# Performance work log

Measured on AMD Instinct MI355X. Metric: run time of the kernel, lower is better.

Reference implementation:

```python
import jax, jax.numpy as jnp
import numpy as np

N_NODES = 50000
HIDDEN = 256
DEPTH = 6
NUM_GRAPHS = 500


def _build_graph(n):
    # 4-regular directed graph: node i -> (i+1, i-1, i+5, i-5) mod n.
    offs = np.array([1, -1, 5, -5], dtype=np.int64)
    src = np.repeat(np.arange(n, dtype=np.int64), 4)
    dst = (src + np.tile(offs, n)) % n
    # incoming edge ids of node u (edge id = 4*src + offset_index)
    u = np.arange(n, dtype=np.int64)
    incoming = np.stack([4 * ((u - 1) % n) + 0,
                         4 * ((u + 1) % n) + 1,
                         4 * ((u - 5) % n) + 2,
                         4 * ((u + 5) % n) + 3], axis=1)  # [n,4]
    E = 4 * n
    pred = incoming[src]           # [E,4] candidate line-graph predecessors of edge e
    pred_src = pred // 4           # source node of each predecessor edge
    keep = pred_src != dst[:, None]  # drop backtracking edge (exactly 1 per row)
    lg_src = pred[keep]                                   # [3E]
    lg_dst = np.repeat(np.arange(E, dtype=np.int64), 4)[keep.ravel()]  # [3E]
    return src, dst, lg_src, lg_dst


def setup_inputs() -> dict:
    key = jax.random.key(0)
    ks = jax.random.split(key, 8)
    n, H = N_NODES, HIDDEN
    E = 4 * n
    _, dst, lg_src, lg_dst = _build_graph(n)
    graph_ids = np.arange(n, dtype=np.int64) // (n // NUM_GRAPHS)
    s = 0.02  # small weight scale keeps relu message passing stable over DEPTH iters
    return {
        "x_nodes": jax.random.normal(ks[0], (n, 35), jnp.float32),
        "x_edges": jax.random.normal(ks[1], (E, 40), jnp.float32),
        "t_m": jax.random.normal(ks[2], (E, H), jnp.float32) * 0.1,
        "W_i": jax.random.normal(ks[3], (40, H), jnp.float32) * s,
        "W_h": jax.random.normal(ks[4], (H, H), jnp.float32) * s,
        "W_o": jax.random.normal(ks[5], (35 + H, H), jnp.float32) * s,
        "b_o": jax.random.normal(ks[6], (H,), jnp.float32) * s,
        "edge_dst": jnp.asarray(dst, jnp.int32),
        "lg_src": jnp.asarray(lg_src, jnp.int32),
        "lg_dst": jnp.asarray(lg_dst, jnp.int32),
        "graph_ids": jnp.asarray(graph_ids, jnp.int32),
        "num_graphs": NUM_GRAPHS,
    }


def reference(x_nodes, x_edges, t_m, W_i, W_h, W_o, b_o,
              edge_dst, lg_src, lg_dst, graph_ids, num_graphs):
    E = x_edges.shape[0]
    n = x_nodes.shape[0]
    binput = x_edges @ W_i                       # W_i has no bias
    g_m = jax.nn.relu(binput)                    # [E,H] per-edge message
    # tree-message aggregation over line graph is constant across depth iters
    t_agg = jax.ops.segment_sum(t_m[lg_src], lg_dst, num_segments=E)
    for _ in range(DEPTH - 1):
        g_agg = jax.ops.segment_sum(g_m[lg_src], lg_dst, num_segments=E)
        g_m = jax.nn.relu(binput + (g_agg + t_agg) @ W_h)
    # edge -> dst-node aggregation (copy_e + sum)
    nei1 = jax.ops.segment_sum(g_m, edge_dst, num_segments=n)
    nei2 = jax.ops.segment_sum(t_m, edge_dst, num_segments=n)
    ainput = jnp.concatenate([x_nodes, nei1 + nei2], axis=1)  # [n, 35+H]
    atom_hiddens = jax.nn.relu(ainput @ W_o + b_o)
    # dgl.mean_nodes: per-graph mean of node features
    sums = jax.ops.segment_sum(atom_hiddens, graph_ids, num_segments=num_graphs)
    counts = jax.ops.segment_sum(jnp.ones((n, 1), atom_hiddens.dtype), graph_ids,
                                 num_segments=num_graphs)
    return sums / counts
```

## Files before the change

kernel.cpp:

```cpp
#include <hip/hip_runtime.h>


#define H 256

typedef __attribute__((ext_vector_type(4))) float f32x4;
typedef __attribute__((ext_vector_type(8))) short bf16x8;

#define MFMA(a, b, c) __builtin_amdgcn_mfma_f32_16x16x32_bf16((a), (b), (c), 0, 0, 0)

__device__ __forceinline__ float bf2f(ushort u) {
  union { unsigned int i; float f; } v; v.i = ((unsigned int)u) << 16; return v.f;
}
__device__ __forceinline__ ushort f2bf(float f) {
  union { float f; unsigned int i; } v; v.f = f;
  unsigned int i = v.i;
  i += 0x7fffu + ((i >> 16) & 1u);
  return (ushort)(i >> 16);
}

union AFrag { bf16x8 v; ushort u[8]; };

__device__ __forceinline__ int edge_delta(int o) {
  return ((o & 2) ? 5 : 1) * ((o & 1) ? -1 : 1);
}

__device__ __forceinline__ int phi(int L) {
  return (L & ~31) | (((L >> 2) & 1) << 4) | (((L >> 3) & 3) << 2) | (L & 3);
}

__global__ __launch_bounds__(256) void prep_weights_kernel(
    const float* __restrict__ Wh, const float* __restrict__ Wi, const float* __restrict__ Wo,
    ushort* __restrict__ WhF, ushort* __restrict__ WiTF,
    ushort* __restrict__ WoT1, ushort* __restrict__ WoT2) {
  const int nn = blockIdx.x;
  const int t = threadIdx.x;
  const int w = phi(nn);
  const int nfg = w >> 4, l15w = w & 15;
  const int ks = t >> 5, kg = (t >> 3) & 3, i = t & 7;
  WhF[((nfg * 8 + ks) << 9) + ((kg << 4) + l15w) * 8 + i] = f2bf(Wh[t * H + nn]);
  WoT2[nn * H + t] = f2bf(Wo[(35 + t) * H + nn]);
  if (t < 64) {
    WiTF[((nfg * 2 + ks) << 9) + ((kg << 4) + l15w) * 8 + i] =
        (t < 40) ? f2bf(Wi[t * H + nn]) : (ushort)0;
    WoT1[nn * 64 + t] = (t < 35) ? f2bf(Wo[t * H + nn]) : (ushort)0;
  }
}

__global__ __launch_bounds__(256) void sum_tm_kernel(
    const float* __restrict__ t_m, ushort* __restrict__ t3, ushort* __restrict__ t4,
    int n, int useT4) {
  const int idx = blockIdx.x * 256 + threadIdx.x;
  const int s = idx >> 5;
  if (s >= n) return;
  const int cg = (idx & 31) * 8;
  int im1 = s - 1; if (im1 < 0) im1 += n;
  int ip1 = s + 1; if (ip1 >= n) ip1 -= n;
  int im5 = s - 5; if (im5 < 0) im5 += n;
  int ip5 = s + 5; if (ip5 >= n) ip5 -= n;
  const size_t e0 = (size_t)(4 * im1 + 0) * H + cg;
  const size_t e1 = (size_t)(4 * ip1 + 1) * H + cg;
  const size_t e2 = (size_t)(4 * im5 + 2) * H + cg;
  const size_t e3 = (size_t)(4 * ip5 + 3) * H + cg;
  f32x4 v0a = *(const f32x4*)(t_m + e0), v0b = *(const f32x4*)(t_m + e0 + 4);
  f32x4 v1a = *(const f32x4*)(t_m + e1), v1b = *(const f32x4*)(t_m + e1 + 4);
  f32x4 v2a = *(const f32x4*)(t_m + e2), v2b = *(const f32x4*)(t_m + e2 + 4);
  f32x4 v3a = *(const f32x4*)(t_m + e3), v3b = *(const f32x4*)(t_m + e3 + 4);
  f32x4 Sa = v0a + v1a + v2a + v3a;
  f32x4 Sb = v0b + v1b + v2b + v3b;
  f32x4 ra[4] = {Sa - v1a, Sa - v0a, Sa - v3a, Sa - v2a};
  f32x4 rb[4] = {Sb - v1b, Sb - v0b, Sb - v3b, Sb - v2b};
  const int cgs = cg >> 5;
  const int cgk = (cg >> 3) & 3;
#pragma unroll
  for (int o = 0; o < 4; ++o) {
    AFrag a;
#pragma unroll
    for (int i = 0; i < 4; ++i) { a.u[i] = f2bf(ra[o][i]); a.u[4 + i] = f2bf(rb[o][i]); }
    const int e = 4 * s + o;
    *(bf16x8*)(t3 + (((size_t)(e >> 4)) << 12) + (cgs << 9) + (((cgk << 4) + (e & 15)) << 3)) = a.v;
  }
  if (useT4) {
    AFrag a;
#pragma unroll
    for (int i = 0; i < 4; ++i) { a.u[i] = f2bf(Sa[i]); a.u[4 + i] = f2bf(Sb[i]); }
    *(bf16x8*)(t4 + (((size_t)(s >> 4)) << 12) + (cgs << 9) + (((cgk << 4) + (s & 15)) << 3)) = a.v;
  }
}

__global__ __launch_bounds__(1024, 8) void prologue_kernel(
    const float* __restrict__ x_edges, const ushort* __restrict__ t3,
    const ushort* __restrict__ WhF, const ushort* __restrict__ WiTF,
    ushort* __restrict__ tb, ushort* __restrict__ g0, int E, int n) {
  extern __shared__ ushort lds[];
  const int tid = threadIdx.x;
  const int wid = tid >> 6, lane = tid & 63, l15 = lane & 15, kg = lane >> 4;
  const int ch = blockIdx.x & 1;

  {
    const bf16x8* src = (const bf16x8*)(WhF) + ch * 4096;
    bf16x8* dstl = (bf16x8*)lds;
#pragma unroll
    for (int j = 0; j < 4; ++j) dstl[tid + j * 1024] = src[tid + j * 1024];
  }
  __syncthreads();

  const int row0 = ((blockIdx.x >> 1) << 8) + wid * 16;
  if (row0 >= E) return;
  const int r = row0 + l15;
  const size_t blkoff = ((size_t)(row0 >> 4)) << 12;

  const float* xp = x_edges + (size_t)r * 40;
  f32x4 xa0 = *(const f32x4*)(xp + kg * 8);
  f32x4 xa1 = *(const f32x4*)(xp + kg * 8 + 4);
  f32x4 xb0, xb1;
  if (kg == 0) { xb0 = *(const f32x4*)(xp + 32); xb1 = *(const f32x4*)(xp + 36); }

  const ushort* t3r = t3 + blkoff + lane * 8;
  bf16x8 av0 = *(const bf16x8*)(t3r);
  bf16x8 av1 = *(const bf16x8*)(t3r + 512);

  f32x4 acc[8];
#pragma unroll
  for (int i = 0; i < 8; ++i) acc[i] = (f32x4){0.f, 0.f, 0.f, 0.f};

  AFrag bx0, bx1;
#pragma unroll
  for (int i = 0; i < 4; ++i) { bx0.u[i] = f2bf(xa0[i]); bx0.u[4 + i] = f2bf(xa1[i]); }
  if (kg == 0) {
#pragma unroll
    for (int i = 0; i < 4; ++i) { bx1.u[i] = f2bf(xb0[i]); bx1.u[4 + i] = f2bf(xb1[i]); }
  } else {
#pragma unroll
    for (int i = 0; i < 8; ++i) bx1.u[i] = 0;
  }
#pragma unroll
  for (int nf = 0; nf < 8; ++nf) {
    bf16x8 a0 = *(const bf16x8*)(WiTF + (((ch * 8 + nf) * 2 + 0) << 9) + lane * 8);
    acc[nf] = MFMA(a0, bx0.v, acc[nf]);
    bf16x8 a1 = *(const bf16x8*)(WiTF + (((ch * 8 + nf) * 2 + 1) << 9) + lane * 8);
    acc[nf] = MFMA(a1, bx1.v, acc[nf]);
  }

  ushort* gout = g0 + blkoff + ((size_t)(ch * 4) << 9) + lane * 8;
#pragma unroll
  for (int tt = 0; tt < 4; ++tt) {
    AFrag pk;
#pragma unroll
    for (int i = 0; i < 4; ++i) {
      pk.u[i]     = f2bf(fmaxf(acc[2 * tt][i], 0.f));
      pk.u[4 + i] = f2bf(fmaxf(acc[2 * tt + 1][i], 0.f));
    }
    *(bf16x8*)(gout + (tt << 9)) = pk.v;
  }

#pragma unroll
  for (int ks = 0; ks < 8; ++ks) {
    bf16x8 av2;
    if (ks < 6) av2 = *(const bf16x8*)(t3r + (ks + 2) * 512);
#pragma unroll
    for (int nf = 0; nf < 8; ++nf) {
      bf16x8 a = *(const bf16x8*)(lds + ((nf * 8 + ks) << 9) + (lane << 3));
      acc[nf] = MFMA(a, av0, acc[nf]);
    }
    av0 = av1; av1 = av2;
  }

  ushort* tbp = tb + blkoff + ((size_t)(ch * 4) << 9) + lane * 8;
#pragma unroll
  for (int tt = 0; tt < 4; ++tt) {
    AFrag pk;
#pragma unroll
    for (int i = 0; i < 4; ++i) {
      pk.u[i]     = f2bf(acc[2 * tt][i]);
      pk.u[4 + i] = f2bf(acc[2 * tt + 1][i]);
    }
    *(bf16x8*)(tbp + (tt << 9)) = pk.v;
  }
}

__global__ __launch_bounds__(1024, 8) void mp_iter_kernel(
    const ushort* __restrict__ gOld, const ushort* __restrict__ tb,
    const ushort* __restrict__ WhF, ushort* __restrict__ gNew, int E, int n) {
  extern __shared__ ushort lds[];
  const int tid = threadIdx.x;
  const int wid = tid >> 6, lane = tid & 63, l15 = lane & 15, kg = lane >> 4;
  const int ch = blockIdx.x & 1;

  {
    const bf16x8* src = (const bf16x8*)(WhF) + ch * 4096;
    bf16x8* dstl = (bf16x8*)lds;
#pragma unroll
    for (int j = 0; j < 4; ++j) dstl[tid + j * 1024] = src[tid + j * 1024];
  }
  __syncthreads();

  const int row0 = ((blockIdx.x >> 1) << 8) + wid * 16;
  if (row0 >= E) return;
  const int r = row0 + l15;
  const size_t blkoff = ((size_t)(row0 >> 4)) << 12;

  const int s = r >> 2, o = r & 3;
  int sm = s - edge_delta(o);
  if (sm < 0) sm += n; else if (sm >= n) sm -= n;
  const int lam = 4 * sm + o;
  const ushort* gr = gOld + (((size_t)(lam >> 4)) << 12) + (((kg << 4) + (lam & 15)) << 3);

  bf16x8 av0 = *(const bf16x8*)(gr);
  bf16x8 av1 = *(const bf16x8*)(gr + 512);

  f32x4 acc[8];
#pragma unroll
  for (int i = 0; i < 8; ++i) acc[i] = (f32x4){0.f, 0.f, 0.f, 0.f};

#pragma unroll
  for (int ks = 0; ks < 8; ++ks) {
    bf16x8 av2;
    if (ks < 6) av2 = *(const bf16x8*)(gr + (ks + 2) * 512);
#pragma unroll
    for (int nf = 0; nf < 8; ++nf) {
      bf16x8 a = *(const bf16x8*)(lds + ((nf * 8 + ks) << 9) + (lane << 3));
      acc[nf] = MFMA(a, av0, acc[nf]);
    }
    av0 = av1; av1 = av2;
  }

  bf16x8 tbv[4];
  const ushort* tbp = tb + blkoff + ((size_t)(ch * 4) << 9) + lane * 8;
#pragma unroll
  for (int tt = 0; tt < 4; ++tt) tbv[tt] = *(const bf16x8*)(tbp + (tt << 9));

  ushort* gout = gNew + blkoff + ((size_t)(ch * 4) << 9) + lane * 8;
#pragma unroll
  for (int tt = 0; tt < 4; ++tt) {
    AFrag pk;
#pragma unroll
    for (int i = 0; i < 4; ++i) {
      const float G0 = acc[2 * tt][i];
      const float G1 = acc[2 * tt + 1][i];
      const float t0 = G0 + __shfl_xor(G0, 2);
      const float S0 = t0 + __shfl_xor(t0, 1);
      const float t1 = G1 + __shfl_xor(G1, 2);
      const float S1 = t1 + __shfl_xor(t1, 1);
      const float d0 = __shfl_xor(G0, 1);
      const float d1 = __shfl_xor(G1, 1);
      const float v0 = bf2f((ushort)tbv[tt][i])     + (S0 - d0);
      const float v1 = bf2f((ushort)tbv[tt][4 + i]) + (S1 - d1);
      pk.u[i]     = f2bf(fmaxf(v0, 0.f));
      pk.u[4 + i] = f2bf(fmaxf(v1, 0.f));
    }
    *(bf16x8*)(gout + (tt << 9)) = pk.v;
  }
}

__global__ __launch_bounds__(256, 3) void readout_kernel(
    const float* __restrict__ x_nodes, const float* __restrict__ t_m,
    const ushort* __restrict__ gP, const ushort* __restrict__ t4,
    const float* __restrict__ b_o,
    const ushort* __restrict__ WoT1, const ushort* __restrict__ WoT2,
    float* __restrict__ out, int n, int npg, int useT4, int bpg) {
  const int gidx = blockIdx.x / bpg;
  const int sub  = blockIdx.x - gidx * bpg;
  const int wid = threadIdx.x >> 6;
  const int lane = threadIdx.x & 63;
  const int l15 = lane & 15;
  const int kg = lane >> 4;
  const int mf = sub * 4 + wid;
  const int rl0 = mf * 16;
  if (rl0 >= npg) return;
  const int u0 = gidx * npg;
  const int rl = rl0 + l15;
  const bool mv = rl < npg;
  const int u = u0 + (mv ? rl : 0);

  int inc[4];
  inc[0] = 4 * ((u - 1 + n) % n);
  inc[1] = 4 * ((u + 1) % n) + 1;
  inc[2] = 4 * ((u - 5 + n) % n) + 2;
  inc[3] = 4 * ((u + 5) % n) + 3;

  f32x4 acc[16];
#pragma unroll
  for (int i = 0; i < 16; ++i) acc[i] = (f32x4){0.f, 0.f, 0.f, 0.f};

#pragma unroll
  for (int ks = 0; ks < 2; ++ks) {
    const int k = ks * 32 + kg * 8;
    AFrag a;
#pragma unroll
    for (int i = 0; i < 8; ++i) {
      const int kk = k + i;
      a.u[i] = (mv && kk < 35) ? f2bf(x_nodes[(size_t)u * 35 + kk]) : (ushort)0;
    }
#pragma unroll
    for (int nf = 0; nf < 16; ++nf) {
      bf16x8 b = *(const bf16x8*)(WoT1 + (nf * 16 + l15) * 64 + k);
      acc[nf] = MFMA(a.v, b, acc[nf]);
    }
  }

#pragma unroll
  for (int ks = 0; ks < 8; ++ks) {
    const int k = ks * 32 + kg * 8;
    AFrag a;
    if (mv) {
      float s[8];
#pragma unroll
      for (int i = 0; i < 8; ++i) s[i] = 0.f;
#pragma unroll
      for (int j = 0; j < 4; ++j) {
        const int e = inc[j];
        const ushort* gp = gP + (((size_t)(e >> 4)) << 12) + ((size_t)ks << 9)
                         + (((kg << 4) + (e & 15)) << 3);
        bf16x8 gv = *(const bf16x8*)gp;
#pragma unroll
        for (int i = 0; i < 8; ++i) s[i] += bf2f((ushort)gv[i]);
      }
      if (useT4) {
        const ushort* tp4 = t4 + (((size_t)(u >> 4)) << 12) + ((size_t)ks << 9)
                          + (((kg << 4) + (u & 15)) << 3);
        bf16x8 tv = *(const bf16x8*)tp4;
#pragma unroll
        for (int i = 0; i < 8; ++i) s[i] += bf2f((ushort)tv[i]);
      } else {
#pragma unroll
        for (int j = 0; j < 4; ++j) {
          const float* tp = t_m + (size_t)inc[j] * H + k;
          f32x4 t0 = *(const f32x4*)tp;
          f32x4 t1 = *(const f32x4*)(tp + 4);
#pragma unroll
          for (int i = 0; i < 4; ++i) { s[i] += t0[i]; s[4 + i] += t1[i]; }
        }
      }
#pragma unroll
      for (int i = 0; i < 8; ++i) a.u[i] = f2bf(s[i]);
    } else {
#pragma unroll
      for (int i = 0; i < 8; ++i) a.u[i] = 0;
    }
#pragma unroll
    for (int nf = 0; nf < 16; ++nf) {
      bf16x8 b = *(const bf16x8*)(WoT2 + (nf * 16 + l15) * H + k);
      acc[nf] = MFMA(a.v, b, acc[nf]);
    }
  }

  const float inv = 1.0f / (float)npg;
#pragma unroll
  for (int nf = 0; nf < 16; ++nf) {
    const int col = nf * 16 + l15;
    const float bias = b_o[col];
    float cs = 0.f;
#pragma unroll
    for (int j = 0; j < 4; ++j) {
      const int rr = rl0 + kg * 4 + j;
      if (rr < npg) cs += fmaxf(acc[nf][j] + bias, 0.f);
    }
    cs += __shfl_xor(cs, 16);
    cs += __shfl_xor(cs, 32);
    if (kg == 0) atomicAdd(&out[(size_t)gidx * H + col], cs * inv);
  }
}

extern "C" void kernel_launch(void* const* d_in, const int* in_sizes, int n_in,
                              void* d_out, int out_size, void* d_ws, size_t ws_size,
                              hipStream_t stream) {
  const float* x_nodes = (const float*)d_in[0];
  const float* x_edges = (const float*)d_in[1];
  const float* t_m     = (const float*)d_in[2];
  const float* W_i     = (const float*)d_in[3];
  const float* W_h     = (const float*)d_in[4];
  const float* W_o     = (const float*)d_in[5];
  const float* b_o     = (const float*)d_in[6];
  (void)n_in;

  const int n = in_sizes[0] / 35;
  const int E = in_sizes[1] / 40;
  const int num_graphs = out_size / H;
  const int npg = n / num_graphs;

  char* ws = (char*)d_ws;
  ushort* WhF  = (ushort*)(ws);
  ushort* WiTF = (ushort*)(ws + 131072);
  ushort* WoT1 = (ushort*)(ws + 164 * 1024);
  ushort* WoT2 = (ushort*)(ws + 200 * 1024);
  size_t off = 336 * 1024;
  const size_t gbytes = (size_t)E * H * 2;
  ushort* tb = (ushort*)(ws + off); off += gbytes;
  ushort* gA = (ushort*)(ws + off); off += gbytes;
  ushort* gB = (ushort*)(ws + off); off += gbytes;
  ushort* t3 = gB;
  const size_t t4bytes = (size_t)n * H * 2;
  const int useT4 = (ws_size >= off + t4bytes) ? 1 : 0;
  ushort* t4 = (ushort*)(ws + off);

  const int nch = (E + 255) >> 8;
  const int bpg = (npg + 63) / 64;

  prep_weights_kernel<<<256, 256, 0, stream>>>(W_h, W_i, W_o, WhF, WiTF, WoT1, WoT2);
  sum_tm_kernel<<<(n * 32 + 255) / 256, 256, 0, stream>>>(t_m, t3, t4, n, useT4);
  prologue_kernel<<<2 * nch, 1024, 65536, stream>>>(x_edges, t3, WhF, WiTF, tb, gA, E, n);

  ushort* src = gA;
  ushort* dst = gB;
  for (int it = 0; it < 5; ++it) {
    mp_iter_kernel<<<2 * nch, 1024, 65536, stream>>>(src, tb, WhF, dst, E, n);
    ushort* tmp = src; src = dst; dst = tmp;
  }

  hipMemsetAsync(d_out, 0, (size_t)out_size * sizeof(float), stream);
  readout_kernel<<<num_graphs * bpg, 256, 0, stream>>>(x_nodes, t_m, src, t4, b_o,
                                                       WoT1, WoT2, (float*)d_out,
                                                       n, npg, useT4, bpg);
}
```

Baseline: 752.6 us.

## Restructure readout: fragment-packed Wo, prefetched gathers, per-neighbor MFMA accumulation

Wo weights are now pre-packed into the MFMA fragment layout, so each lane reads its B operand with one contiguous 16-byte load. The readout no longer sums the four incoming edge messages plus the t4 row in fp32 and rounds to bf16. It feeds each gathered bf16 row straight into its own MFMA, which multiplies MFMA work by up to five but removes the conversion and add ALU work. Gathers for the next k-slice are software-prefetched so the irregular loads overlap the current MFMAs. Rows with no valid node are no longer zeroed on the t4 path, which relies on clamped indices and the later row mask.

Measured after the change: 757.4 us. No clear change (+0.6%).

```diff
diff --git a/kernel.cpp b/kernel.cpp
--- a/kernel.cpp
+++ b/kernel.cpp
@@ -31,18 +31,24 @@
 __global__ __launch_bounds__(256) void prep_weights_kernel(
     const float* __restrict__ Wh, const float* __restrict__ Wi, const float* __restrict__ Wo,
     ushort* __restrict__ WhF, ushort* __restrict__ WiTF,
-    ushort* __restrict__ WoT1, ushort* __restrict__ WoT2) {
+    ushort* __restrict__ WoT1F, ushort* __restrict__ WoT2F) {
   const int nn = blockIdx.x;
   const int t = threadIdx.x;
-  const int w = phi(nn);
-  const int nfg = w >> 4, l15w = w & 15;
   const int ks = t >> 5, kg = (t >> 3) & 3, i = t & 7;
-  WhF[((nfg * 8 + ks) << 9) + ((kg << 4) + l15w) * 8 + i] = f2bf(Wh[t * H + nn]);
-  WoT2[nn * H + t] = f2bf(Wo[(35 + t) * H + nn]);
-  if (t < 64) {
-    WiTF[((nfg * 2 + ks) << 9) + ((kg << 4) + l15w) * 8 + i] =
-        (t < 40) ? f2bf(Wi[t * H + nn]) : (ushort)0;
-    WoT1[nn * 64 + t] = (t < 35) ? f2bf(Wo[t * H + nn]) : (ushort)0;
+  {
+    const int w = phi(nn);
+    const int nfg = w >> 4, l15w = w & 15;
+    WhF[((nfg * 8 + ks) << 9) + ((kg << 4) + l15w) * 8 + i] = f2bf(Wh[t * H + nn]);
+    if (t < 64)
+      WiTF[((nfg * 2 + ks) << 9) + ((kg << 4) + l15w) * 8 + i] =
+          (t < 40) ? f2bf(Wi[t * H + nn]) : (ushort)0;
+  }
+  {
+    const int nf = nn >> 4, l15 = nn & 15;
+    WoT2F[((nf * 8 + ks) << 9) + ((kg << 4) + l15) * 8 + i] = f2bf(Wo[(35 + t) * H + nn]);
+    if (t < 64)
+      WoT1F[((nf * 2 + ks) << 9) + ((kg << 4) + l15) * 8 + i] =
+          (t < 35) ? f2bf(Wo[t * H + nn]) : (ushort)0;
   }
 }
 
@@ -256,7 +262,7 @@
     const float* __restrict__ x_nodes, const float* __restrict__ t_m,
     const ushort* __restrict__ gP, const ushort* __restrict__ t4,
     const float* __restrict__ b_o,
-    const ushort* __restrict__ WoT1, const ushort* __restrict__ WoT2,
+    const ushort* __restrict__ WoT1F, const ushort* __restrict__ WoT2F,
     float* __restrict__ out, int n, int npg, int useT4, int bpg) {
   const int gidx = blockIdx.x / bpg;
   const int sub  = blockIdx.x - gidx * bpg;
@@ -278,9 +284,22 @@
   inc[2] = 4 * ((u - 5 + n) % n) + 2;
   inc[3] = 4 * ((u + 5) % n) + 3;
 
+  const ushort* gsrc0 = gP + (((size_t)(inc[0] >> 4)) << 12) + (((kg << 4) + (inc[0] & 15)) << 3);
+  const ushort* gsrc1 = gP + (((size_t)(inc[1] >> 4)) << 12) + (((kg << 4) + (inc[1] & 15)) << 3);
+  const ushort* gsrc2 = gP + (((size_t)(inc[2] >> 4)) << 12) + (((kg << 4) + (inc[2] & 15)) << 3);
+  const ushort* gsrc3 = gP + (((size_t)(inc[3] >> 4)) << 12) + (((kg << 4) + (inc[3] & 15)) << 3);
+  const ushort* t4p   = t4 + (((size_t)(u >> 4)) << 12) + (((kg << 4) + (u & 15)) << 3);
+
   f32x4 acc[16];
 #pragma unroll
   for (int i = 0; i < 16; ++i) acc[i] = (f32x4){0.f, 0.f, 0.f, 0.f};
+
+  bf16x8 c0 = *(const bf16x8*)(gsrc0);
+  bf16x8 c1 = *(const bf16x8*)(gsrc1);
+  bf16x8 c2 = *(const bf16x8*)(gsrc2);
+  bf16x8 c3 = *(const bf16x8*)(gsrc3);
+  bf16x8 c4;
+  if (useT4) c4 = *(const bf16x8*)(t4p);
 
 #pragma unroll
   for (int ks = 0; ks < 2; ++ks) {
@@ -293,55 +312,54 @@
     }
 #pragma unroll
     for (int nf = 0; nf < 16; ++nf) {
-      bf16x8 b = *(const bf16x8*)(WoT1 + (nf * 16 + l15) * 64 + k);
+      bf16x8 b = *(const bf16x8*)(WoT1F + ((nf * 2 + ks) << 9) + (lane << 3));
       acc[nf] = MFMA(a.v, b, acc[nf]);
     }
   }
 
 #pragma unroll
   for (int ks = 0; ks < 8; ++ks) {
-    const int k = ks * 32 + kg * 8;
-    AFrag a;
-    if (mv) {
+    bf16x8 n0, n1, n2, n3, n4;
+    if (ks < 7) {
+      const int koff = (ks + 1) * 512;
+      n0 = *(const bf16x8*)(gsrc0 + koff);
+      n1 = *(const bf16x8*)(gsrc1 + koff);
+      n2 = *(const bf16x8*)(gsrc2 + koff);
+      n3 = *(const bf16x8*)(gsrc3 + koff);
+      if (useT4) n4 = *(const bf16x8*)(t4p + koff);
+    }
+    AFrag ex;
+    if (!useT4) {
+      const int k = ks * 32 + kg * 8;
       float s[8];
 #pragma unroll
       for (int i = 0; i < 8; ++i) s[i] = 0.f;
-#pragma unroll
-      for (int j = 0; j < 4; ++j) {
-        const int e = inc[j];
-        const ushort* gp = gP + (((size_t)(e >> 4)) << 12) + ((size_t)ks << 9)
-                         + (((kg << 4) + (e & 15)) << 3);
-        bf16x8 gv = *(const bf16x8*)gp;
-#pragma unroll
-        for (int i = 0; i < 8; ++i) s[i] += bf2f((ushort)gv[i]);
-      }
-      if (useT4) {
-        const ushort* tp4 = t4 + (((size_t)(u >> 4)) << 12) + ((size_t)ks << 9)
-                          + (((kg << 4) + (u & 15)) << 3);
-        bf16x8 tv = *(const bf16x8*)tp4;
-#pragma unroll
-        for (int i = 0; i < 8; ++i) s[i] += bf2f((ushort)tv[i]);
-      } else {
+      if (mv) {
 #pragma unroll
         for (int j = 0; j < 4; ++j) {
           const float* tp = t_m + (size_t)inc[j] * H + k;
-          f32x4 t0 = *(const f32x4*)tp;
-          f32x4 t1 = *(const f32x4*)(tp + 4);
-#pragma unroll
-          for (int i = 0; i < 4; ++i) { s[i] += t0[i]; s[4 + i] += t1[i]; }
+          f32x4 q0 = *(const f32x4*)tp;
+          f32x4 q1 = *(const f32x4*)(tp + 4);
+#pragma unroll
+          for (int i = 0; i < 4; ++i) { s[i] += q0[i]; s[4 + i] += q1[i]; }
         }
       }
 #pragma unroll
-      for (int i = 0; i < 8; ++i) a.u[i] = f2bf(s[i]);
-    } else {
-#pragma unroll
-      for (int i = 0; i < 8; ++i) a.u[i] = 0;
+      for (int i = 0; i < 8; ++i) ex.u[i] = f2bf(s[i]);
     }
 #pragma unroll
     for (int nf = 0; nf < 16; ++nf) {
-      bf16x8 b = *(const bf16x8*)(WoT2 + (nf * 16 + l15) * H + k);
-      acc[nf] = MFMA(a.v, b, acc[nf]);
-    }
+      bf16x8 b = *(const bf16x8*)(WoT2F + ((nf * 8 + ks) << 9) + (lane << 3));
+      f32x4 t = MFMA(c0, b, acc[nf]);
+      t = MFMA(c1, b, t);
+      t = MFMA(c2, b, t);
+      t = MFMA(c3, b, t);
+      if (useT4) t = MFMA(c4, b, t);
+      else       t = MFMA(ex.v, b, t);
+      acc[nf] = t;
+    }
+    c0 = n0; c1 = n1; c2 = n2; c3 = n3;
+    if (useT4) c4 = n4;
   }
 
   const float inv = 1.0f / (float)npg;
@@ -379,10 +397,10 @@
   const int npg = n / num_graphs;
 
   char* ws = (char*)d_ws;
-  ushort* WhF  = (ushort*)(ws);
-  ushort* WiTF = (ushort*)(ws + 131072);
-  ushort* WoT1 = (ushort*)(ws + 164 * 1024);
-  ushort* WoT2 = (ushort*)(ws + 200 * 1024);
+  ushort* WhF   = (ushort*)(ws);
+  ushort* WiTF  = (ushort*)(ws + 131072);
+  ushort* WoT1F = (ushort*)(ws + 164 * 1024);
+  ushort* WoT2F = (ushort*)(ws + 200 * 1024);
   size_t off = 336 * 1024;
   const size_t gbytes = (size_t)E * H * 2;
   ushort* tb = (ushort*)(ws + off); off += gbytes;
@@ -396,7 +414,7 @@
   const int nch = (E + 255) >> 8;
   const int bpg = (npg + 63) / 64;
 
-  prep_weights_kernel<<<256, 256, 0, stream>>>(W_h, W_i, W_o, WhF, WiTF, WoT1, WoT2);
+  prep_weights_kernel<<<256, 256, 0, stream>>>(W_h, W_i, W_o, WhF, WiTF, WoT1F, WoT2F);
   sum_tm_kernel<<<(n * 32 + 255) / 256, 256, 0, stream>>>(t_m, t3, t4, n, useT4);
   prologue_kernel<<<2 * nch, 1024, 65536, stream>>>(x_edges, t3, WhF, WiTF, tb, gA, E, n);
 
@@ -409,6 +427,6 @@
 
   hipMemsetAsync(d_out, 0, (size_t)out_size * sizeof(float), stream);
   readout_kernel<<<num_graphs * bpg, 256, 0, stream>>>(x_nodes, t_m, src, t4, b_o,
-                                                       WoT1, WoT2, (float*)d_out,
+                                                       WoT1F, WoT2F, (float*)d_out,
                                                        n, npg, useT4, bpg);
 }
```
